# Optimization experiments

Measured on AMD Instinct MI355X. Metric: run time of the kernel, lower is better.

## Reference

```python
import jax, jax.numpy as jnp
import numpy as np

HEADS = 20


def _sdpa(q, k, v):
    # q: [B,H,Sq,D], k/v: [B,H,Sk,D]
    scale = 1.0 / jnp.sqrt(jnp.asarray(q.shape[-1], q.dtype))
    scores = jnp.einsum('bhqd,bhkd->bhqk', q, k) * scale
    probs = jax.nn.softmax(scores, axis=-1)
    return jnp.einsum('bhqk,bhkd->bhqd', probs, v)


def _split_heads(x, B, H):
    # [B,S,H*D] -> [B,H,S,D]
    S = x.shape[1]
    D = x.shape[2] // H
    return x.reshape(B, S, H, D).transpose(0, 2, 1, 3)


def setup_inputs() -> dict:
    key = jax.random.key(0)
    ks = jax.random.split(key, 10)
    B, S, C = 4, 4096, 1280
    T, Lid, X = 77, 32, 2048
    sc = lambda fan_in: 1.0 / np.sqrt(fan_in)
    return {
        'hidden_states': jax.random.normal(ks[0], (B, S, C), jnp.float32),
        'encoder_hidden_states': jax.random.normal(ks[1], (B, T, X), jnp.float32),
        'id_embedding': jax.random.normal(ks[2], (B, Lid, X), jnp.float32),
        'Wq': jax.random.normal(ks[3], (C, C), jnp.float32) * sc(C),
        'Wk': jax.random.normal(ks[4], (C, X), jnp.float32) * sc(X),
        'Wv': jax.random.normal(ks[5], (C, X), jnp.float32) * sc(X),
        'Wik': jax.random.normal(ks[6], (C, X), jnp.float32) * sc(X),
        'Wiv': jax.random.normal(ks[7], (C, X), jnp.float32) * sc(X),
        'Wo': jax.random.normal(ks[8], (C, C), jnp.float32) * sc(C),
        'bo': jnp.zeros((C,), jnp.float32),
    }


def reference(hidden_states, encoder_hidden_states, id_embedding,
              Wq, Wk, Wv, Wik, Wiv, Wo, bo):
    id_scale = 1.0
    B, S, C = hidden_states.shape
    H = HEADS
    residual = hidden_states

    q = _split_heads(hidden_states @ Wq.T, B, H)              # [B,H,S,D]
    k = _split_heads(encoder_hidden_states @ Wk.T, B, H)      # [B,H,T,D]
    v = _split_heads(encoder_hidden_states @ Wv.T, B, H)

    cross = _sdpa(q, k, v)                                    # [B,H,S,D]

    id_k = _split_heads(id_embedding @ Wik.T, B, H)           # [B,H,Lid,D]
    id_v = _split_heads(id_embedding @ Wiv.T, B, H)
    id_out = _sdpa(q, id_k, id_v)                             # [B,H,S,D]

    combined = cross + id_scale * id_out
    combined = combined.transpose(0, 2, 1, 3).reshape(B, S, C)

    out = combined @ Wo.T + bo
    out = out + residual  # residual_connection=True, rescale_output_factor=1.0
    return out
```

## Files before the change

### kernel.cpp

```cpp
#include <hip/hip_runtime.h>

typedef short short8 __attribute__((ext_vector_type(8)));
typedef unsigned short ushort8 __attribute__((ext_vector_type(8)));
typedef float float4v __attribute__((ext_vector_type(4)));

__device__ __forceinline__ unsigned short f2bf(float f) {
    union { float f; unsigned u; } v; v.f = f;
    unsigned r = v.u + 0x7fffu + ((v.u >> 16) & 1u);
    return (unsigned short)(r >> 16);
}

__device__ __forceinline__ void async_copy16(const void* g, void* l) {
    __builtin_amdgcn_global_load_lds(
        (__attribute__((address_space(1))) void*)g,
        (__attribute__((address_space(3))) void*)l,
        16, 0, 0);
}

__global__ __launch_bounds__(256) void cast_bf16_kernel(
        const float* __restrict__ in, unsigned short* __restrict__ out, int n) {
    int i4 = (blockIdx.x * 256 + threadIdx.x) * 4;
    if (i4 < n) {
        float4 f = *(const float4*)(in + i4);
        ushort4 u;
        u.x = f2bf(f.x); u.y = f2bf(f.y); u.z = f2bf(f.z); u.w = f2bf(f.w);
        *(ushort4*)(out + i4) = u;
    }
}

__global__ __launch_bounds__(256) void cast_enc_pad_kernel(
        const float* __restrict__ in, unsigned short* __restrict__ out) {
    int i4 = blockIdx.x * 256 + threadIdx.x;
    if (i4 < 4 * 77 * 2048 / 4) {
        const int per_b = 77 * 2048 / 4;
        int b = i4 / per_b;
        int rem = i4 - b * per_b;
        float4 f = *(const float4*)(in + (size_t)i4 * 4);
        ushort4 u;
        u.x = f2bf(f.x); u.y = f2bf(f.y); u.z = f2bf(f.z); u.w = f2bf(f.w);
        *(ushort4*)(out + ((size_t)b * (96 * 2048 / 4) + rem) * 4) = u;
    }
}

struct CastBatch {
    const float* src[8];
    unsigned short* dst[8];
    int n[8];
};
__global__ __launch_bounds__(256) void cast_batch_kernel(CastBatch cb) {
    const int t = blockIdx.y;
    const int n = cb.n[t];
    int i4 = (blockIdx.x * 256 + threadIdx.x) * 4;
    if (i4 < n) {
        float4 f = *(const float4*)(cb.src[t] + i4);
        ushort4 u;
        u.x = f2bf(f.x); u.y = f2bf(f.y); u.z = f2bf(f.z); u.w = f2bf(f.w);
        *(ushort4*)(cb.dst[t] + i4) = u;
    }
}

__global__ __launch_bounds__(256) void gemm_kv4_kernel(
        const unsigned short* __restrict__ Aenc,
        const unsigned short* __restrict__ Aid,
        const unsigned short* __restrict__ Wk,
        const unsigned short* __restrict__ Wv,
        const unsigned short* __restrict__ Wik,
        const unsigned short* __restrict__ Wiv,
        unsigned short* __restrict__ Kb, unsigned short* __restrict__ Vb,
        unsigned short* __restrict__ IKb, unsigned short* __restrict__ IVb,
        int N, int K) {
    const int z = blockIdx.z;
    const int bm = blockIdx.x * 64;
    const int Mrows = (z < 2) ? 384 : 128;
    if (bm >= Mrows) return;
    const unsigned short* A = (z < 2) ? Aenc : Aid;
    const unsigned short* B = (z == 0) ? Wk : (z == 1) ? Wv : (z == 2) ? Wik : Wiv;
    unsigned short* C = (z == 0) ? Kb : (z == 1) ? Vb : (z == 2) ? IKb : IVb;
    const int bn = blockIdx.y * 128;

    __shared__ unsigned short As[64 * 64];
    __shared__ unsigned short Bs[128 * 64];

    const int tid  = threadIdx.x;
    const int lane = tid & 63;
    const int wave = tid >> 6;
    const int wm   = (wave >> 1) * 32;
    const int wn   = (wave & 1) * 64;
    const int lr   = lane & 15;
    const int lq   = lane >> 4;

    float4v acc[2][4] = {};

    const unsigned short* aptr[2];
    const unsigned short* bptr[4];
    #pragma unroll
    for (int r = 0; r < 2; ++r) {
        const int linear = r * 256 + tid;
        const int row = linear >> 3;
        const int c = (linear & 7) ^ (row & 7);
        aptr[r] = A + (size_t)(bm + row) * K + c * 8;
    }
    #pragma unroll
    for (int r = 0; r < 4; ++r) {
        const int linear = r * 256 + tid;
        const int row = linear >> 3;
        const int c = (linear & 7) ^ (row & 7);
        bptr[r] = B + (size_t)(bn + row) * K + c * 8;
    }

    for (int ks = 0; ks < K; ks += 64) {
        #pragma unroll
        for (int r = 0; r < 2; ++r)
            async_copy16(aptr[r] + ks, (char*)As + (size_t)(r * 256 + tid) * 16);
        #pragma unroll
        for (int r = 0; r < 4; ++r)
            async_copy16(bptr[r] + ks, (char*)Bs + (size_t)(r * 256 + tid) * 16);
        __syncthreads();

        #pragma unroll
        for (int kw = 0; kw < 2; ++kw) {
            short8 af[2], bfr[4];
            #pragma unroll
            for (int i = 0; i < 2; ++i) {
                const int row = wm + i * 16 + lr;
                af[i] = *(const short8*)(As + row * 64 + (((kw << 2) | lq) ^ (row & 7)) * 8);
            }
            #pragma unroll
            for (int j = 0; j < 4; ++j) {
                const int row = wn + j * 16 + lr;
                bfr[j] = *(const short8*)(Bs + row * 64 + (((kw << 2) | lq) ^ (row & 7)) * 8);
            }
            #pragma unroll
            for (int i = 0; i < 2; ++i)
                #pragma unroll
                for (int j = 0; j < 4; ++j)
                    acc[i][j] = __builtin_amdgcn_mfma_f32_16x16x32_bf16(
                                    af[i], bfr[j], acc[i][j], 0, 0, 0);
        }
        __syncthreads();
    }

    #pragma unroll
    for (int i = 0; i < 2; ++i) {
        #pragma unroll
        for (int r = 0; r < 4; ++r) {
            const int row = bm + wm + i * 16 + lq * 4 + r;
            const size_t base = (size_t)row * N;
            #pragma unroll
            for (int j = 0; j < 4; ++j) {
                const int col = bn + wn + j * 16 + lr;
                C[base + col] = f2bf(acc[i][j][r]);
            }
        }
    }
}

template<int EPI>
__global__ __launch_bounds__(512) void gemm256_kernel(
        const unsigned short* __restrict__ A,
        const unsigned short* __restrict__ B,
        float* __restrict__ Cf,
        unsigned short* __restrict__ Cb,
        const float* __restrict__ bias,
        const float* __restrict__ resid,
        int N, int K, int tn) {
    __shared__ unsigned short As[2][256 * 64];
    __shared__ unsigned short Bs[2][256 * 64];

    const int tid  = threadIdx.x;
    const int lane = tid & 63;
    const int wave = tid >> 6;
    const int wm   = (wave >> 2) * 128;
    const int wn   = (wave & 3) * 64;
    const int l15  = lane & 15;
    const int lq   = lane >> 4;

    int wg = blockIdx.x;
    const int q = gridDim.x >> 3;
    wg = (wg & 7) * q + (wg >> 3);
    const int mt = wg / tn;
    const int nt = wg - mt * tn;
    const int bm = mt * 256;
    const int bn = nt * 256;

    float4v acc[8][4] = {};

    const unsigned short* aptr[4];
    const unsigned short* bptr[4];
    #pragma unroll
    for (int r = 0; r < 4; ++r) {
        const int linear = r * 512 + tid;
        const int row = linear >> 3;
        const int c = (linear & 7) ^ (row & 7);
        aptr[r] = A + (size_t)(bm + row) * K + c * 8;
        bptr[r] = B + (size_t)(bn + row) * K + c * 8;
    }

    auto stage = [&](int ks, int b) {
        #pragma unroll
        for (int r = 0; r < 4; ++r)
            async_copy16(aptr[r] + ks, (char*)&As[b][0] + (r * 512 + tid) * 16);
        #pragma unroll
        for (int r = 0; r < 4; ++r)
            async_copy16(bptr[r] + ks, (char*)&Bs[b][0] + (r * 512 + tid) * 16);
    };

    const int NT = K >> 6;
    stage(0, 0);
    stage(64, 1);

    for (int t = 0; t < NT; ++t) {
        const int cur = t & 1;
        if (t == NT - 1) {
            asm volatile("s_waitcnt vmcnt(0)" ::: "memory");
        } else {
            asm volatile("s_waitcnt vmcnt(8)" ::: "memory");
        }
        __builtin_amdgcn_s_barrier();
        __builtin_amdgcn_sched_barrier(0);

        short8 a0[8], b0[4], a1[8], b1[4];
        #pragma unroll
        for (int i = 0; i < 8; ++i) {
            const int row = wm + i * 16 + l15;
            a0[i] = *(const short8*)(&As[cur][row * 64 + ((lq ^ (row & 7)) << 3)]);
        }
        #pragma unroll
        for (int j = 0; j < 4; ++j) {
            const int row = wn + j * 16 + l15;
            b0[j] = *(const short8*)(&Bs[cur][row * 64 + ((lq ^ (row & 7)) << 3)]);
        }
        #pragma unroll
        for (int i = 0; i < 8; ++i)
            #pragma unroll
            for (int j = 0; j < 4; ++j)
                acc[i][j] = __builtin_amdgcn_mfma_f32_16x16x32_bf16(
                                a0[i], b0[j], acc[i][j], 0, 0, 0);
        #pragma unroll
        for (int i = 0; i < 8; ++i) {
            const int row = wm + i * 16 + l15;
            a1[i] = *(const short8*)(&As[cur][row * 64 + (((4 | lq) ^ (row & 7)) << 3)]);
        }
        #pragma unroll
        for (int j = 0; j < 4; ++j) {
            const int row = wn + j * 16 + l15;
            b1[j] = *(const short8*)(&Bs[cur][row * 64 + (((4 | lq) ^ (row & 7)) << 3)]);
        }
        asm volatile("s_waitcnt lgkmcnt(0)" ::: "memory");
        __builtin_amdgcn_sched_barrier(0);
        if (t < NT - 2) {
            __builtin_amdgcn_s_barrier();
            stage((t + 2) << 6, cur);
        }
        __builtin_amdgcn_s_setprio(1);
        #pragma unroll
        for (int i = 0; i < 8; ++i)
            #pragma unroll
            for (int j = 0; j < 4; ++j)
                acc[i][j] = __builtin_amdgcn_mfma_f32_16x16x32_bf16(
                                a1[i], b1[j], acc[i][j], 0, 0, 0);
        __builtin_amdgcn_s_setprio(0);
    }

    #pragma unroll
    for (int i = 0; i < 8; ++i) {
        #pragma unroll
        for (int r = 0; r < 4; ++r) {
            const int row = bm + wm + i * 16 + lq * 4 + r;
            const size_t base = (size_t)row * N;
            #pragma unroll
            for (int j = 0; j < 4; ++j) {
                const int col = bn + wn + j * 16 + l15;
                const float v = acc[i][j][r];
                const size_t idx = base + col;
                if (EPI == 2)      Cf[idx] = v + bias[col] + resid[idx];
                else if (EPI == 1) Cb[idx] = f2bf(v);
                else               Cf[idx] = v;
            }
        }
    }
}

#define VT_STRIDE 136
__global__ __launch_bounds__(256) void attn_mfma_kernel(
        const unsigned short* __restrict__ Q,
        const unsigned short* __restrict__ Kb,
        const unsigned short* __restrict__ Vb,
        const unsigned short* __restrict__ IKb,
        const unsigned short* __restrict__ IVb,
        unsigned short* __restrict__ Cmb) {
    const int b = blockIdx.z;
    const int h = blockIdx.y;
    const int hoff = h * 64;
    const int qbase = blockIdx.x * 64;
    const int tid = threadIdx.x;
    const int lane = tid & 63;
    const int wave = tid >> 6;
    const int l15 = lane & 15;
    const int quad = lane >> 4;

    __shared__ unsigned short Vt[64 * VT_STRIDE];
    __shared__ unsigned short Pl[64 * VT_STRIDE];

    for (int i = tid; i < 96 * 8; i += 256) {
        const int c = i / 96;
        const int key = i - c * 96;
        short8 v = *(const short8*)(Vb + (size_t)(b * 96 + key) * 1280 + hoff + c * 8);
        #pragma unroll
        for (int j = 0; j < 8; ++j)
            Vt[(c * 8 + j) * VT_STRIDE + key] = (unsigned short)v[j];
    }
    {
        const int c = tid >> 5;
        const int key = tid & 31;
        short8 v = *(const short8*)(IVb + (size_t)(b * 32 + key) * 1280 + hoff + c * 8);
        #pragma unroll
        for (int j = 0; j < 8; ++j)
            Vt[(c * 8 + j) * VT_STRIDE + 96 + key] = (unsigned short)v[j];
    }
    __syncthreads();

    const int qrow = b * 4096 + qbase + wave * 16 + l15;
    const unsigned short* qp = Q + (size_t)qrow * 1280 + hoff + quad * 8;
    const short8 aQ0 = *(const short8*)(qp);
    const short8 aQ1 = *(const short8*)(qp + 32);

    const float scale = 0.125f;
    float lC[4] = {0.f, 0.f, 0.f, 0.f};
    float lI[4] = {0.f, 0.f, 0.f, 0.f};

    #pragma unroll
    for (int t = 0; t < 5; ++t) {
        const unsigned short* kp = Kb + (size_t)(b * 96 + t * 16 + l15) * 1280 + hoff + quad * 8;
        const short8 bK0 = *(const short8*)(kp);
        const short8 bK1 = *(const short8*)(kp + 32);
        float4v s = {};
        s = __builtin_amdgcn_mfma_f32_16x16x32_bf16(aQ0, bK0, s, 0, 0, 0);
        s = __builtin_amdgcn_mfma_f32_16x16x32_bf16(aQ1, bK1, s, 0, 0, 0);
        #pragma unroll
        for (int r = 0; r < 4; ++r) {
            float p = __expf(s[r] * scale);
            if (t == 4 && l15 >= 13) p = 0.f;
            lC[r] += p;
            Pl[(wave * 16 + quad * 4 + r) * VT_STRIDE + t * 16 + l15] = f2bf(p);
        }
    }
    #pragma unroll
    for (int r = 0; r < 4; ++r)
        Pl[(wave * 16 + quad * 4 + r) * VT_STRIDE + 80 + l15] = 0;

    #pragma unroll
    for (int t = 0; t < 2; ++t) {
        const unsigned short* kp = IKb + (size_t)(b * 32 + t * 16 + l15) * 1280 + hoff + quad * 8;
        const short8 bK0 = *(const short8*)(kp);
        const short8 bK1 = *(const short8*)(kp + 32);
        float4v s = {};
        s = __builtin_amdgcn_mfma_f32_16x16x32_bf16(aQ0, bK0, s, 0, 0, 0);
        s = __builtin_amdgcn_mfma_f32_16x16x32_bf16(aQ1, bK1, s, 0, 0, 0);
        #pragma unroll
        for (int r = 0; r < 4; ++r) {
            const float p = __expf(s[r] * scale);
            lI[r] += p;
            Pl[(wave * 16 + quad * 4 + r) * VT_STRIDE + 96 + t * 16 + l15] = f2bf(p);
        }
    }

    #pragma unroll
    for (int m = 1; m <= 8; m <<= 1) {
        #pragma unroll
        for (int r = 0; r < 4; ++r) {
            lC[r] += __shfl_xor(lC[r], m);
            lI[r] += __shfl_xor(lI[r], m);
        }
    }
    __syncthreads();

    float4v oC[4] = {};
    float4v oI[4] = {};
    #pragma unroll
    for (int kt = 0; kt < 3; ++kt) {
        const short8 aP = *(const short8*)(Pl + (wave * 16 + l15) * VT_STRIDE + kt * 32 + quad * 8);
        #pragma unroll
        for (int td = 0; td < 4; ++td) {
            const short8 bV = *(const short8*)(Vt + (td * 16 + l15) * VT_STRIDE + kt * 32 + quad * 8);
            oC[td] = __builtin_amdgcn_mfma_f32_16x16x32_bf16(aP, bV, oC[td], 0, 0, 0);
        }
    }
    {
        const short8 aP = *(const short8*)(Pl + (wave * 16 + l15) * VT_STRIDE + 96 + quad * 8);
        #pragma unroll
        for (int td = 0; td < 4; ++td) {
            const short8 bV = *(const short8*)(Vt + (td * 16 + l15) * VT_STRIDE + 96 + quad * 8);
            oI[td] = __builtin_amdgcn_mfma_f32_16x16x32_bf16(aP, bV, oI[td], 0, 0, 0);
        }
    }

    float rc[4], ri[4];
    #pragma unroll
    for (int r = 0; r < 4; ++r) { rc[r] = 1.f / lC[r]; ri[r] = 1.f / lI[r]; }

    #pragma unroll
    for (int td = 0; td < 4; ++td) {
        #pragma unroll
        for (int r = 0; r < 4; ++r) {
            const int row = b * 4096 + qbase + wave * 16 + quad * 4 + r;
            const int col = hoff + td * 16 + l15;
            Cmb[(size_t)row * 1280 + col] = f2bf(oC[td][r] * rc[r] + oI[td][r] * ri[r]);
        }
    }
}

extern "C" void kernel_launch(void* const* d_in, const int* in_sizes, int n_in,
                              void* d_out, int out_size, void* d_ws, size_t ws_size,
                              hipStream_t stream) {
    const float* hs  = (const float*)d_in[0];
    const float* enc = (const float*)d_in[1];
    const float* idm = (const float*)d_in[2];
    const float* Wq  = (const float*)d_in[3];
    const float* Wk  = (const float*)d_in[4];
    const float* Wv  = (const float*)d_in[5];
    const float* Wik = (const float*)d_in[6];
    const float* Wiv = (const float*)d_in[7];
    const float* Wo  = (const float*)d_in[8];
    const float* bo  = (const float*)d_in[9];
    float* out = (float*)d_out;

    char* ws = (char*)d_ws;
    size_t off = 0;
    auto carve = [&](size_t bytes) {
        char* p = ws + off;
        off += (bytes + 255) & ~(size_t)255;
        return p;
    };

    unsigned short* Xh   = (unsigned short*)carve(16384ULL * 1280 * 2);
    unsigned short* Wq_b = (unsigned short*)carve(1280ULL * 1280 * 2);
    unsigned short* Wk_b = (unsigned short*)carve(1280ULL * 2048 * 2);
    unsigned short* Wv_b = (unsigned short*)carve(1280ULL * 2048 * 2);
    unsigned short* Wik_b= (unsigned short*)carve(1280ULL * 2048 * 2);
    unsigned short* Wiv_b= (unsigned short*)carve(1280ULL * 2048 * 2);
    unsigned short* Wo_b = (unsigned short*)carve(1280ULL * 1280 * 2);
    unsigned short* Encb = (unsigned short*)carve(384ULL * 2048 * 2);
    unsigned short* Idb  = (unsigned short*)carve(128ULL * 2048 * 2);
    unsigned short* Qb   = (unsigned short*)carve(16384ULL * 1280 * 2);
    unsigned short* Kb   = (unsigned short*)carve(384ULL * 1280 * 2);
    unsigned short* Vb   = (unsigned short*)carve(384ULL * 1280 * 2);
    unsigned short* IKb  = (unsigned short*)carve(128ULL * 1280 * 2);
    unsigned short* IVb  = (unsigned short*)carve(128ULL * 1280 * 2);
    (void)ws_size; (void)in_sizes; (void)n_in; (void)out_size;

    cast_bf16_kernel<<<(4 * 4096 * 1280 / 4 + 255) / 256, 256, 0, stream>>>(
        hs, Xh, 4 * 4096 * 1280);
    cast_enc_pad_kernel<<<(4 * 77 * 2048 / 4 + 255) / 256, 256, 0, stream>>>(enc, Encb);

    CastBatch cb;
    cb.src[0] = Wq;  cb.dst[0] = Wq_b;  cb.n[0] = 1280 * 1280;
    cb.src[1] = Wk;  cb.dst[1] = Wk_b;  cb.n[1] = 1280 * 2048;
    cb.src[2] = Wv;  cb.dst[2] = Wv_b;  cb.n[2] = 1280 * 2048;
    cb.src[3] = Wik; cb.dst[3] = Wik_b; cb.n[3] = 1280 * 2048;
    cb.src[4] = Wiv; cb.dst[4] = Wiv_b; cb.n[4] = 1280 * 2048;
    cb.src[5] = Wo;  cb.dst[5] = Wo_b;  cb.n[5] = 1280 * 1280;
    cb.src[6] = idm; cb.dst[6] = Idb;   cb.n[6] = 4 * 32 * 2048;
    cb.src[7] = nullptr; cb.dst[7] = nullptr; cb.n[7] = 0;
    cast_batch_kernel<<<dim3((1280 * 2048 / 4 + 255) / 256, 7), 256, 0, stream>>>(cb);

    gemm256_kernel<1><<<dim3(64 * 5), 512, 0, stream>>>(
        Xh, Wq_b, nullptr, Qb, nullptr, nullptr, 1280, 1280, 5);

    gemm_kv4_kernel<<<dim3(6, 10, 4), 256, 0, stream>>>(
        Encb, Idb, Wk_b, Wv_b, Wik_b, Wiv_b, Kb, Vb, IKb, IVb, 1280, 2048);

    attn_mfma_kernel<<<dim3(64, 20, 4), 256, 0, stream>>>(Qb, Kb, Vb, IKb, IVb, Xh);

    gemm256_kernel<2><<<dim3(64 * 5), 512, 0, stream>>>(
        Xh, Wo_b, out, nullptr, bo, hs, 1280, 1280, 5);
}
```

Baseline: 461.8 us.

## Retile large GEMMs to 256x320 blocks with K-step 32 and two blocks per CU

The Q and output projection GEMMs move from 256x256 tiles with a K-step of 64 to 256x320 tiles with a K-step of 32. This drops the grid from 320 to 256 workgroups, so one wave of blocks fits the 256 CUs evenly. The change adds a new LDS swizzle, per-wave staging counts, and launch bounds that ask for two blocks per CU. Each wave now holds 40 accumulators instead of 32, which raises register pressure, and the shorter K-step means more barriers per K.

```diff
diff --git a/kernel.cpp b/kernel.cpp
--- a/kernel.cpp
+++ b/kernel.cpp
@@ -156,7 +156,7 @@
 }
 
 template<int EPI>
-__global__ __launch_bounds__(512) void gemm256_kernel(
+__global__ __launch_bounds__(512, 2) void gemm320_kernel(
         const unsigned short* __restrict__ A,
         const unsigned short* __restrict__ B,
         float* __restrict__ Cf,
@@ -164,14 +164,14 @@
         const float* __restrict__ bias,
         const float* __restrict__ resid,
         int N, int K, int tn) {
-    __shared__ unsigned short As[2][256 * 64];
-    __shared__ unsigned short Bs[2][256 * 64];
+    __shared__ unsigned short As[2][256 * 32];
+    __shared__ unsigned short Bs[2][320 * 32];
 
     const int tid  = threadIdx.x;
     const int lane = tid & 63;
     const int wave = tid >> 6;
-    const int wm   = (wave >> 2) * 128;
-    const int wn   = (wave & 3) * 64;
+    const int wm   = (wave >> 1) * 64;
+    const int wn   = (wave & 1) * 160;
     const int l15  = lane & 15;
     const int lq   = lane >> 4;
 
@@ -181,95 +181,96 @@
     const int mt = wg / tn;
     const int nt = wg - mt * tn;
     const int bm = mt * 256;
-    const int bn = nt * 256;
-
-    float4v acc[8][4] = {};
-
-    const unsigned short* aptr[4];
-    const unsigned short* bptr[4];
-    #pragma unroll
-    for (int r = 0; r < 4; ++r) {
-        const int linear = r * 512 + tid;
-        const int row = linear >> 3;
-        const int c = (linear & 7) ^ (row & 7);
-        aptr[r] = A + (size_t)(bm + row) * K + c * 8;
-        bptr[r] = B + (size_t)(bn + row) * K + c * 8;
-    }
-
-    auto stage = [&](int ks, int b) {
-        #pragma unroll
-        for (int r = 0; r < 4; ++r)
-            async_copy16(aptr[r] + ks, (char*)&As[b][0] + (r * 512 + tid) * 16);
-        #pragma unroll
-        for (int r = 0; r < 4; ++r)
-            async_copy16(bptr[r] + ks, (char*)&Bs[b][0] + (r * 512 + tid) * 16);
+    const int bn = nt * 320;
+
+    float4v acc[4][10] = {};
+
+    const unsigned short* aS[2];
+    const unsigned short* bS[2];
+    const unsigned short* bS2;
+    int dA[2], dB[2], dB2;
+    #pragma unroll
+    for (int g = 0; g < 2; ++g) {
+        const int d = g * 512 + tid;
+        const int row = d >> 2;
+        const int c = (d & 3) ^ ((row >> 1) & 3);
+        aS[g] = A + (size_t)(bm + row) * K + c * 8;
+        bS[g] = B + (size_t)(bn + row) * K + c * 8;
+        dA[g] = d * 16;
+        dB[g] = d * 16;
+    }
+    {
+        const int t2 = tid & 255;
+        const int d = 1024 + t2;
+        const int row = d >> 2;
+        const int c = (d & 3) ^ ((row >> 1) & 3);
+        bS2 = B + (size_t)(bn + row) * K + c * 8;
+        dB2 = d * 16;
+    }
+
+    auto stage = [&](int t) {
+        const int b = t & 1;
+        #pragma unroll
+        for (int g = 0; g < 2; ++g)
+            async_copy16(aS[g] + t * 32, (char*)&As[b][0] + dA[g]);
+        #pragma unroll
+        for (int g = 0; g < 2; ++g)
+            async_copy16(bS[g] + t * 32, (char*)&Bs[b][0] + dB[g]);
+        if (wave < 4)
+            async_copy16(bS2 + t * 32, (char*)&Bs[b][0] + dB2);
     };
 
-    const int NT = K >> 6;
-    stage(0, 0);
-    stage(64, 1);
+    const int NT = K >> 5;
+    stage(0);
+    stage(1);
 
     for (int t = 0; t < NT; ++t) {
         const int cur = t & 1;
         if (t == NT - 1) {
             asm volatile("s_waitcnt vmcnt(0)" ::: "memory");
+        } else if (wave < 4) {
+            asm volatile("s_waitcnt vmcnt(5)" ::: "memory");
         } else {
-            asm volatile("s_waitcnt vmcnt(8)" ::: "memory");
+            asm volatile("s_waitcnt vmcnt(4)" ::: "memory");
         }
         __builtin_amdgcn_s_barrier();
         __builtin_amdgcn_sched_barrier(0);
 
-        short8 a0[8], b0[4], a1[8], b1[4];
-        #pragma unroll
-        for (int i = 0; i < 8; ++i) {
+        short8 af[4], bf[10];
+        #pragma unroll
+        for (int i = 0; i < 4; ++i) {
             const int row = wm + i * 16 + l15;
-            a0[i] = *(const short8*)(&As[cur][row * 64 + ((lq ^ (row & 7)) << 3)]);
-        }
-        #pragma unroll
-        for (int j = 0; j < 4; ++j) {
+            af[i] = *(const short8*)(&As[cur][row * 32 + ((lq ^ ((row >> 1) & 3)) << 3)]);
+        }
+        #pragma unroll
+        for (int j = 0; j < 10; ++j) {
             const int row = wn + j * 16 + l15;
-            b0[j] = *(const short8*)(&Bs[cur][row * 64 + ((lq ^ (row & 7)) << 3)]);
-        }
-        #pragma unroll
-        for (int i = 0; i < 8; ++i)
-            #pragma unroll
-            for (int j = 0; j < 4; ++j)
-                acc[i][j] = __builtin_amdgcn_mfma_f32_16x16x32_bf16(
-                                a0[i], b0[j], acc[i][j], 0, 0, 0);
-        #pragma unroll
-        for (int i = 0; i < 8; ++i) {
-            const int row = wm + i * 16 + l15;
-            a1[i] = *(const short8*)(&As[cur][row * 64 + (((4 | lq) ^ (row & 7)) << 3)]);
-        }
-        #pragma unroll
-        for (int j = 0; j < 4; ++j) {
-            const int row = wn + j * 16 + l15;
-            b1[j] = *(const short8*)(&Bs[cur][row * 64 + (((4 | lq) ^ (row & 7)) << 3)]);
+            bf[j] = *(const short8*)(&Bs[cur][row * 32 + ((lq ^ ((row >> 1) & 3)) << 3)]);
         }
         asm volatile("s_waitcnt lgkmcnt(0)" ::: "memory");
         __builtin_amdgcn_sched_barrier(0);
         if (t < NT - 2) {
             __builtin_amdgcn_s_barrier();
-            stage((t + 2) << 6, cur);
+            stage(t + 2);
         }
         __builtin_amdgcn_s_setprio(1);
         #pragma unroll
-        for (int i = 0; i < 8; ++i)
-            #pragma unroll
-            for (int j = 0; j < 4; ++j)
+        for (int i = 0; i < 4; ++i)
+            #pragma unroll
+            for (int j = 0; j < 10; ++j)
                 acc[i][j] = __builtin_amdgcn_mfma_f32_16x16x32_bf16(
-                                a1[i], b1[j], acc[i][j], 0, 0, 0);
+                                af[i], bf[j], acc[i][j], 0, 0, 0);
         __builtin_amdgcn_s_setprio(0);
     }
 
     #pragma unroll
-    for (int i = 0; i < 8; ++i) {
+    for (int i = 0; i < 4; ++i) {
         #pragma unroll
         for (int r = 0; r < 4; ++r) {
             const int row = bm + wm + i * 16 + lq * 4 + r;
             const size_t base = (size_t)row * N;
             #pragma unroll
-            for (int j = 0; j < 4; ++j) {
+            for (int j = 0; j < 10; ++j) {
                 const int col = bn + wn + j * 16 + l15;
                 const float v = acc[i][j][r];
                 const size_t idx = base + col;
@@ -464,14 +465,14 @@
     cb.src[7] = nullptr; cb.dst[7] = nullptr; cb.n[7] = 0;
     cast_batch_kernel<<<dim3((1280 * 2048 / 4 + 255) / 256, 7), 256, 0, stream>>>(cb);
 
-    gemm256_kernel<1><<<dim3(64 * 5), 512, 0, stream>>>(
-        Xh, Wq_b, nullptr, Qb, nullptr, nullptr, 1280, 1280, 5);
+    gemm320_kernel<1><<<dim3(64 * 4), 512, 0, stream>>>(
+        Xh, Wq_b, nullptr, Qb, nullptr, nullptr, 1280, 1280, 4);
 
     gemm_kv4_kernel<<<dim3(6, 10, 4), 256, 0, stream>>>(
         Encb, Idb, Wk_b, Wv_b, Wik_b, Wiv_b, Kb, Vb, IKb, IVb, 1280, 2048);
 
     attn_mfma_kernel<<<dim3(64, 20, 4), 256, 0, stream>>>(Qb, Kb, Vb, IKb, IVb, Xh);
 
-    gemm256_kernel<2><<<dim3(64 * 5), 512, 0, stream>>>(
-        Xh, Wo_b, out, nullptr, bo, hs, 1280, 1280, 5);
-}
+    gemm320_kernel<2><<<dim3(64 * 4), 512, 0, stream>>>(
+        Xh, Wo_b, out, nullptr, bo, hs, 1280, 1280, 4);
+}
```

After: 423.7 us. 1.09x faster.
